# Performance work log

Measured on AMD Instinct MI355X. Metric: run time of the kernel, lower is better.

## Reference

```python
import jax, jax.numpy as jnp
import numpy as np

# SO(2)-equivariant linear (eSCN, arXiv:2302.03655), 'uv' fully-connected mode.
# Irreps l = 0..4 on both input and output sides.
LS = (0, 1, 2, 3, 4)
N, C_IN, C_OUT = 8192, 128, 128


def _build_paths():
    """Enumerate sparse-product entries (in_idx, out_idx, weight_idx, coef).

    Per (l_in, l_out) path: one weight for m=0, and for each 1<=m<=min(l_in,l_out)
    a (w_re, w_im) pair acting as the 2x2 rotation
        y_{+m} = w_re x_{+m} - w_im x_{-m}
        y_{-m} = w_im x_{+m} + w_re x_{-m}
    path_norm scales every path into an output irrep by 1/sqrt(#paths).
    """
    dims = [2 * l + 1 for l in LS]
    off = np.concatenate([[0], np.cumsum(dims)[:-1]])  # start of each irrep block
    pn = 1.0 / np.sqrt(len(LS))  # every output irrep receives len(LS) paths
    in_idx, out_idx, w_idx, coef = [], [], [], []
    w = 0
    for lo_i, lo in enumerate(LS):
        for li_i, li in enumerate(LS):
            oi, oo = int(off[li_i]), int(off[lo_i])
            # m = 0 component (index l within a (2l+1) block)
            in_idx.append(oi + li); out_idx.append(oo + lo); w_idx.append(w); coef.append(pn)
            w += 1
            for m in range(1, min(li, lo) + 1):
                ip, im = oi + li + m, oi + li - m   # input +m / -m positions
                op, om = oo + lo + m, oo + lo - m   # output +m / -m positions
                w_re, w_im = w, w + 1
                w += 2
                for ii, jj, ww, s in ((ip, op, w_re, 1.0), (im, om, w_re, 1.0),
                                      (ip, om, w_im, 1.0), (im, op, w_im, -1.0)):
                    in_idx.append(ii); out_idx.append(jj); w_idx.append(ww); coef.append(s * pn)
    return (np.asarray(in_idx), np.asarray(out_idx), np.asarray(w_idx),
            np.asarray(coef, np.float32), w, int(sum(dims)))


IN_IDX, OUT_IDX, W_IDX, COEF, NUM_W, DIM = _build_paths()  # NUM_W=85, DIM=25, T=145


def setup_inputs() -> dict:
    key = jax.random.key(0)
    k1, k2 = jax.random.split(key)
    x = jax.random.normal(k1, (N, DIM, C_IN), jnp.float32)
    wgt = jax.random.normal(k2, (NUM_W, C_IN, C_OUT), jnp.float32) * (C_IN ** -0.5)
    return {"input": x, "weight": wgt}


def reference(input, weight):
    coef = jnp.asarray(COEF)
    # gather one row per sparse-product entry: [N, T, C_in]
    x = input[:, IN_IDX, :] * coef[None, :, None]
    # per-entry vec-mat with the entry's weight matrix: [N, T, C_out]
    y = jnp.einsum('ntc,tcd->ntd', x, weight[W_IDX])
    # scatter-add entries into their output irrep components
    out = jnp.zeros((input.shape[0], DIM, weight.shape[-1]), y.dtype)
    return out.at[:, OUT_IDX, :].add(y)
```

## Files before the change

kernel.cpp:

```cpp
#include <hip/hip_runtime.h>
#include <cstdint>
#include <cstddef>

#define NROWS 8192
#define DIM   25
#define CIN   128
#define COUT  128
#define MAXT  160

struct Tables {
  int   w_idx[MAXT];
  float coef[MAXT];
  int   o_start[DIM + 1];
  int   e_in[MAXT];
  int   e_t[MAXT];
  int   T;
};

constexpr Tables build_tables() {
  Tables tb{};
  int off[5] = {0, 1, 4, 9, 16};
  const float pn = 0.44721359549995793f;
  int in_idx[MAXT] = {}, out_idx[MAXT] = {}, widx[MAXT] = {};
  float cf[MAXT] = {};
  int T = 0, w = 0;
  for (int lo = 0; lo < 5; ++lo) {
    for (int li = 0; li < 5; ++li) {
      int oi = off[li], oo = off[lo];
      in_idx[T] = oi + li; out_idx[T] = oo + lo; widx[T] = w; cf[T] = pn; ++T; ++w;
      int mm = li < lo ? li : lo;
      for (int m = 1; m <= mm; ++m) {
        int ip = oi + li + m, im = oi + li - m;
        int op = oo + lo + m, om = oo + lo - m;
        int wre = w, wim = w + 1; w += 2;
        in_idx[T] = ip; out_idx[T] = op; widx[T] = wre; cf[T] = pn;  ++T;
        in_idx[T] = im; out_idx[T] = om; widx[T] = wre; cf[T] = pn;  ++T;
        in_idx[T] = ip; out_idx[T] = om; widx[T] = wim; cf[T] = pn;  ++T;
        in_idx[T] = im; out_idx[T] = op; widx[T] = wim; cf[T] = -pn; ++T;
      }
    }
  }
  tb.T = T;
  for (int t = 0; t < T; ++t) { tb.w_idx[t] = widx[t]; tb.coef[t] = cf[t]; }
  int pos = 0;
  for (int o = 0; o < DIM; ++o) {
    tb.o_start[o] = pos;
    for (int t = 0; t < T; ++t)
      if (out_idx[t] == o) { tb.e_in[pos] = in_idx[t]; tb.e_t[pos] = t; ++pos; }
  }
  tb.o_start[DIM] = pos;
  return tb;
}

__constant__ Tables TAB = build_tables();

__device__ __forceinline__ uint16_t f2bf(float f) {
  uint32_t u = __float_as_uint(f);
  uint32_t r = (u + 0x7FFFu + ((u >> 16) & 1u)) >> 16;
  return (uint16_t)r;
}

__device__ __forceinline__ void load_lds16(const void* g, void* l) {
  __builtin_amdgcn_global_load_lds(
      (const __attribute__((address_space(1))) uint32_t*)g,
      (__attribute__((address_space(3))) uint32_t*)l, 16, 0, 0);
}

typedef __bf16 v8bf __attribute__((ext_vector_type(8)));
typedef float  v4f  __attribute__((ext_vector_type(4)));

__global__ void cvt_kernel(const float* __restrict__ X, uint16_t* __restrict__ Y,
                           int n4) {
  int i = blockIdx.x * blockDim.x + threadIdx.x;
  if (i < n4) {
    float4 v = ((const float4*)X)[i];
    ushort4 o;
    o.x = f2bf(v.x); o.y = f2bf(v.y); o.z = f2bf(v.z); o.w = f2bf(v.w);
    ((ushort4*)Y)[i] = o;
  }
}

__global__ void prepw_kernel(const float* __restrict__ W, uint16_t* __restrict__ Bt) {
  int t = blockIdx.x;
  int w = TAB.w_idx[t];
  float cf = TAB.coef[t];
  const float* Wp = W + (size_t)w * CIN * COUT;
  uint16_t* Bp = Bt + (size_t)t * CIN * COUT;
  for (int idx = threadIdx.x; idx < CIN * COUT; idx += blockDim.x) {
    int d = idx >> 7, c = idx & 127;
    Bp[idx] = f2bf(cf * Wp[(size_t)c * COUT + d]);
  }
}

__global__ __launch_bounds__(256) void so2_gemm(
    const uint16_t* __restrict__ Xb,
    const uint16_t* __restrict__ Bt,
    float* __restrict__ Out) {
  __shared__ __align__(16) uint16_t As[128 * 64];
  __shared__ __align__(16) uint16_t Bs[128 * 64];

  const int o  = blockIdx.x;
  const int n0 = blockIdx.y << 7;
  const int e0 = TAB.o_start[o];
  const int nE = TAB.o_start[o + 1] - e0;

  const int tid  = threadIdx.x;
  const int w    = tid >> 6;
  const int l    = tid & 63;

  const int srow = (w << 3) + (l >> 3);
  const int slot = l & 7;
  const int ssrc = ((slot ^ (l >> 3)) << 3);

  const int lr   = l & 15;
  const int quad = l >> 4;
  const int wr   = (w & 1) << 6;
  const int wc   = (w >> 1) << 6;

  v4f acc[4][4];
  #pragma unroll
  for (int i = 0; i < 4; ++i)
    #pragma unroll
    for (int j = 0; j < 4; ++j)
      acc[i][j] = v4f{0.f, 0.f, 0.f, 0.f};

  const int nIter = nE << 1;
  for (int ki = 0; ki < nIter; ++ki) {
    const int e    = e0 + (ki >> 1);
    const int kk   = (ki & 1) << 6;
    const int irow = TAB.e_in[e];
    const int trow = TAB.e_t[e];

    const uint16_t* gA = Xb + ((size_t)(n0 + srow) * DIM + irow) * CIN + kk + ssrc;
    const uint16_t* gB = Bt + ((size_t)trow * COUT + srow) * CIN + kk + ssrc;

    if (ki) __syncthreads();
    #pragma unroll
    for (int j = 0; j < 4; ++j) {
      const int m = (j << 5) + srow;
      load_lds16(gA + (size_t)(j << 5) * (DIM * CIN), &As[m * 64 + slot * 8]);
      load_lds16(gB + (size_t)(j << 5) * CIN,         &Bs[m * 64 + slot * 8]);
    }
    __syncthreads();

    #pragma unroll
    for (int kk2 = 0; kk2 < 2; ++kk2) {
      const int s = (((kk2 << 2) + quad) ^ (lr & 7)) << 3;
      v8bf a[4], b[4];
      #pragma unroll
      for (int i = 0; i < 4; ++i) {
        a[i] = *(const v8bf*)(&As[(wr + (i << 4) + lr) * 64 + s]);
        b[i] = *(const v8bf*)(&Bs[(wc + (i << 4) + lr) * 64 + s]);
      }
      #pragma unroll
      for (int i = 0; i < 4; ++i)
        #pragma unroll
        for (int j = 0; j < 4; ++j)
          acc[i][j] = __builtin_amdgcn_mfma_f32_16x16x32_bf16(a[i], b[j],
                                                              acc[i][j], 0, 0, 0);
    }
  }

  #pragma unroll
  for (int i = 0; i < 4; ++i) {
    #pragma unroll
    for (int r = 0; r < 4; ++r) {
      const int n = n0 + wr + (i << 4) + (quad << 2) + r;
      float* op = Out + ((size_t)n * DIM + o) * COUT + wc + lr;
      #pragma unroll
      for (int j = 0; j < 4; ++j)
        op[j << 4] = acc[i][j][r];
    }
  }
}

extern "C" void kernel_launch(void* const* d_in, const int* in_sizes, int n_in,
                              void* d_out, int out_size, void* d_ws, size_t ws_size,
                              hipStream_t stream) {
  const float* X = (const float*)d_in[0];
  const float* W = (const float*)d_in[1];
  float* Out = (float*)d_out;

  uint16_t* Xb = (uint16_t*)d_ws;
  uint16_t* Bt = (uint16_t*)((char*)d_ws + (size_t)NROWS * DIM * CIN * 2);

  {
    int n4 = NROWS * DIM * CIN / 4;
    int blocks = (n4 + 255) / 256;
    cvt_kernel<<<blocks, 256, 0, stream>>>(X, Xb, n4);
  }
  prepw_kernel<<<145, 256, 0, stream>>>(W, Bt);
  {
    dim3 grid(DIM, NROWS / 128);
    so2_gemm<<<grid, 256, 0, stream>>>(Xb, Bt, Out);
  }
}
```

Baseline: 261.7 us.

## Merge prep kernels and remap GEMM blocks so each XCD shares row tiles

Folds the activation bf16 conversion and the weight transpose/scale into a single launch, removing one kernel launch and the gap between them. The GEMM grid becomes 1D and is remapped so that blocks on the same XCD (lb & 7) handle the same 128-row tiles across all 25 output components. Those blocks then reuse the same gathered input rows in that XCD's L2. The intent is to cut launch overhead and duplicated HBM reads of X. The mapping depends on round-robin XCD dispatch, which is an assumption about scheduling.

```diff
diff --git a/kernel.cpp b/kernel.cpp
--- a/kernel.cpp
+++ b/kernel.cpp
@@ -69,26 +69,26 @@
 typedef __bf16 v8bf __attribute__((ext_vector_type(8)));
 typedef float  v4f  __attribute__((ext_vector_type(4)));
 
-__global__ void cvt_kernel(const float* __restrict__ X, uint16_t* __restrict__ Y,
-                           int n4) {
-  int i = blockIdx.x * blockDim.x + threadIdx.x;
-  if (i < n4) {
+#define NCVT (NROWS * DIM * CIN / 4 / 256)
+
+__global__ void prep_kernel(const float* __restrict__ X, uint16_t* __restrict__ Y,
+                            const float* __restrict__ W, uint16_t* __restrict__ Bt) {
+  if (blockIdx.x < NCVT) {
+    int i = blockIdx.x * 256 + threadIdx.x;
     float4 v = ((const float4*)X)[i];
     ushort4 o;
     o.x = f2bf(v.x); o.y = f2bf(v.y); o.z = f2bf(v.z); o.w = f2bf(v.w);
     ((ushort4*)Y)[i] = o;
-  }
-}
-
-__global__ void prepw_kernel(const float* __restrict__ W, uint16_t* __restrict__ Bt) {
-  int t = blockIdx.x;
-  int w = TAB.w_idx[t];
-  float cf = TAB.coef[t];
-  const float* Wp = W + (size_t)w * CIN * COUT;
-  uint16_t* Bp = Bt + (size_t)t * CIN * COUT;
-  for (int idx = threadIdx.x; idx < CIN * COUT; idx += blockDim.x) {
-    int d = idx >> 7, c = idx & 127;
-    Bp[idx] = f2bf(cf * Wp[(size_t)c * COUT + d]);
+  } else {
+    int t = blockIdx.x - NCVT;
+    int w = TAB.w_idx[t];
+    float cf = TAB.coef[t];
+    const float* Wp = W + (size_t)w * CIN * COUT;
+    uint16_t* Bp = Bt + (size_t)t * CIN * COUT;
+    for (int idx = threadIdx.x; idx < CIN * COUT; idx += blockDim.x) {
+      int d = idx >> 7, c = idx & 127;
+      Bp[idx] = f2bf(cf * Wp[(size_t)c * COUT + d]);
+    }
   }
 }
 
@@ -99,8 +99,13 @@
   __shared__ __align__(16) uint16_t As[128 * 64];
   __shared__ __align__(16) uint16_t Bs[128 * 64];
 
-  const int o  = blockIdx.x;
-  const int n0 = blockIdx.y << 7;
+  const int lb   = blockIdx.x;
+  const int xcd  = lb & 7;
+  const int slot = lb >> 3;
+  const int o    = slot % 25;
+  const int nt   = xcd + ((slot / 25) << 3);
+  const int n0   = nt << 7;
+
   const int e0 = TAB.o_start[o];
   const int nE = TAB.o_start[o + 1] - e0;
 
@@ -109,8 +114,8 @@
   const int l    = tid & 63;
 
   const int srow = (w << 3) + (l >> 3);
-  const int slot = l & 7;
-  const int ssrc = ((slot ^ (l >> 3)) << 3);
+  const int slt  = l & 7;
+  const int ssrc = ((slt ^ (l >> 3)) << 3);
 
   const int lr   = l & 15;
   const int quad = l >> 4;
@@ -138,8 +143,8 @@
     #pragma unroll
     for (int j = 0; j < 4; ++j) {
       const int m = (j << 5) + srow;
-      load_lds16(gA + (size_t)(j << 5) * (DIM * CIN), &As[m * 64 + slot * 8]);
-      load_lds16(gB + (size_t)(j << 5) * CIN,         &Bs[m * 64 + slot * 8]);
+      load_lds16(gA + (size_t)(j << 5) * (DIM * CIN), &As[m * 64 + slt * 8]);
+      load_lds16(gB + (size_t)(j << 5) * CIN,         &Bs[m * 64 + slt * 8]);
     }
     __syncthreads();
 
@@ -184,14 +189,6 @@
   uint16_t* Xb = (uint16_t*)d_ws;
   uint16_t* Bt = (uint16_t*)((char*)d_ws + (size_t)NROWS * DIM * CIN * 2);
 
-  {
-    int n4 = NROWS * DIM * CIN / 4;
-    int blocks = (n4 + 255) / 256;
-    cvt_kernel<<<blocks, 256, 0, stream>>>(X, Xb, n4);
-  }
-  prepw_kernel<<<145, 256, 0, stream>>>(W, Bt);
-  {
-    dim3 grid(DIM, NROWS / 128);
-    so2_gemm<<<grid, 256, 0, stream>>>(Xb, Bt, Out);
-  }
+  prep_kernel<<<NCVT + 145, 256, 0, stream>>>(X, Xb, W, Bt);
+  so2_gemm<<<DIM * (NROWS / 128), 256, 0, stream>>>(Xb, Bt, Out);
 }
```

New measurement: 273.8 us. 1.05x slower.
